# Optimization experiments

Measured on AMD Instinct MI355X. Metric: run time of the kernel, lower is better.

## Reference

```python
import jax, jax.numpy as jnp
import numpy as np

B, T, D, N = 2, 2048, 2048, 16
H = D // N          # 128 head dim
F = H // 2          # 64 rotary frequencies


def setup_inputs() -> dict:
    key = jax.random.key(0)
    k1, k2, k3 = jax.random.split(key, 3)
    x = jax.random.normal(k1, (B, T, D), dtype=jnp.float32)
    # causal mask [T, T], True = attend
    mask = jnp.tril(jnp.ones((T, T), dtype=bool))
    # RoPE tables: freqs = 1 / 10000^(2i/H), angles = t * freqs
    freqs = 1.0 / (10000.0 ** (jnp.arange(0, H, 2, dtype=jnp.float32) / H))  # [F]
    angles = jnp.arange(T, dtype=jnp.float32)[:, None] * freqs[None, :]      # [T, F]
    cos, sin = jnp.cos(angles), jnp.sin(angles)
    w_attn = jax.random.normal(k2, (D, 3 * D), dtype=jnp.float32) * 0.02
    w_out = jax.random.normal(k3, (D, D), dtype=jnp.float32) * 0.02
    return {"x": x, "mask": mask, "cos": cos, "sin": sin,
            "w_attn": w_attn, "w_out": w_out}


def _rope(x_BNTH, cos_TF, sin_TF):
    # complex multiply on adjacent pairs of the head dim
    x = x_BNTH.reshape(*x_BNTH.shape[:-1], F, 2)  # [B,N,T,F,2]
    xr, xi = x[..., 0], x[..., 1]
    out_r = xr * cos_TF - xi * sin_TF             # broadcast [T,F] over [B,N,T,F]
    out_i = xr * sin_TF + xi * cos_TF
    return jnp.stack([out_r, out_i], axis=-1).reshape(x_BNTH.shape)


def reference(x, mask, cos, sin, w_attn, w_out):
    qkv = x @ w_attn                                  # [B,T,3D]
    q, k, v = jnp.split(qkv, 3, axis=-1)
    def to_heads(z):
        return z.reshape(B, T, N, H).transpose(0, 2, 1, 3)  # [B,N,T,H]
    q, k, v = to_heads(q), to_heads(k), to_heads(v)
    # NOTE: this module applies rotary embedding to k AND v (not q), per source
    k = _rope(k, cos, sin)
    v = _rope(v, cos, sin)
    scale = 1.0 / jnp.sqrt(jnp.asarray(H, dtype=q.dtype))
    scores = jnp.einsum('bnqh,bnkh->bnqk', q, k) * scale  # [B,N,T,T]
    scores = jnp.where(mask, scores, jnp.finfo(scores.dtype).min)
    attn = jax.nn.softmax(scores, axis=-1)
    o = jnp.einsum('bnqk,bnkh->bnqh', attn, v)            # [B,N,T,H]
    o = o.transpose(0, 2, 1, 3).reshape(B, T, D)          # [B,T,D]
    return o @ w_out
```

## Files before the change

### kernel.cpp

```cpp
#include <hip/hip_runtime.h>

typedef unsigned short u16;
typedef unsigned int u32;

#define B_ 2
#define T_ 2048
#define D_ 2048
#define N_ 16
#define H_ 128
#define F_ 64
#define SCALE 0.08838834764831845f

typedef __attribute__((ext_vector_type(8))) __bf16 bf16x8;
typedef __attribute__((ext_vector_type(8))) short s16x8;
typedef __attribute__((ext_vector_type(4))) float f32x4;
typedef __attribute__((ext_vector_type(4))) u16 u16x4;

__device__ inline u16 f2bf(float f) {
    union { float f; u32 u; } v; v.f = f;
    u32 u = v.u;
    u32 r = (u + 0x7FFFu + ((u >> 16) & 1u)) >> 16;
    return (u16)r;
}
__device__ inline float bf2f(u16 h) {
    union { u32 u; float f; } v; v.u = ((u32)h) << 16;
    return v.f;
}
__device__ inline bf16x8 ld8(const u16* p) {
    s16x8 r = *reinterpret_cast<const s16x8*>(p);
    return __builtin_bit_cast(bf16x8, r);
}
__device__ inline f32x4 mfma16(bf16x8 a, bf16x8 b, f32x4 c) {
    return __builtin_amdgcn_mfma_f32_16x16x32_bf16(a, b, c, 0, 0, 0);
}
__device__ inline void gload_lds16(const u16* g, u16* l) {
    __builtin_amdgcn_global_load_lds(
        (const __attribute__((address_space(1))) void*)g,
        (__attribute__((address_space(3))) void*)l, 16, 0, 0);
}

__global__ __launch_bounds__(256) void cvt_bf16(const float* __restrict__ in,
                                                u16* __restrict__ out, int n) {
    int i = (blockIdx.x * 256 + threadIdx.x) * 8;
    if (i >= n) return;
    float4 a = *reinterpret_cast<const float4*>(in + i);
    float4 b = *reinterpret_cast<const float4*>(in + i + 4);
    s16x8 o;
    o[0] = (short)f2bf(a.x); o[1] = (short)f2bf(a.y);
    o[2] = (short)f2bf(a.z); o[3] = (short)f2bf(a.w);
    o[4] = (short)f2bf(b.x); o[5] = (short)f2bf(b.y);
    o[6] = (short)f2bf(b.z); o[7] = (short)f2bf(b.w);
    *reinterpret_cast<s16x8*>(out + i) = o;
}

__global__ __launch_bounds__(256) void transpose_cvt(const float* __restrict__ in,
                                                     u16* __restrict__ out,
                                                     int K, int Nc) {
    __shared__ float tile[64][65];
    int n0 = blockIdx.x * 64, k0 = blockIdx.y * 64;
    int tid = threadIdx.x;
    int rr = tid >> 4;
    int cc = (tid & 15) * 4;
#pragma unroll
    for (int it = 0; it < 4; ++it) {
        int kk = it * 16 + rr;
        float4 v = *reinterpret_cast<const float4*>(in + (size_t)(k0 + kk) * Nc + n0 + cc);
        tile[kk][cc] = v.x; tile[kk][cc + 1] = v.y; tile[kk][cc + 2] = v.z; tile[kk][cc + 3] = v.w;
    }
    __syncthreads();
#pragma unroll
    for (int it = 0; it < 4; ++it) {
        int nn = it * 16 + rr;
        u16x4 o;
#pragma unroll
        for (int j = 0; j < 4; ++j) o[j] = f2bf(tile[cc + j][nn]);
        *reinterpret_cast<u16x4*>(out + (size_t)(n0 + nn) * K + k0 + cc) = o;
    }
}

#define BM 128
#define BN 128
#define BKg 32

__global__ __launch_bounds__(256) void gemm_bt(const u16* __restrict__ A,
                                               const u16* __restrict__ Bt,
                                               u16* __restrict__ Cb,
                                               float* __restrict__ Cf,
                                               int M, int Nn, int K, int out_f32) {
    __shared__ __align__(16) u16 As[2][BM * BKg];
    __shared__ __align__(16) u16 Bs[2][BM * BKg];
    const int tid = threadIdx.x;
    const int wave = tid >> 6, lane = tid & 63;
    const int m0 = blockIdx.y * BM, n0 = blockIdx.x * BN;
    const int lrow = lane >> 2, lcol = (lane & 3) * 8;
    const int wr = (wave >> 1) * 64, wc = (wave & 1) * 64;
    const int g = lane >> 4, c0 = lane & 15;

    f32x4 acc[4][4] = {};

    const int NT = K / BKg;

    auto stage = [&](int buf, int kt) {
        const int k0 = kt * BKg;
#pragma unroll
        for (int j = 0; j < 2; ++j) {
            const int c = wave + j * 4;
            gload_lds16(A + (size_t)(m0 + c * 16 + lrow) * K + k0 + lcol, &As[buf][c * 512]);
            gload_lds16(Bt + (size_t)(n0 + c * 16 + lrow) * K + k0 + lcol, &Bs[buf][c * 512]);
        }
    };

    stage(0, 0);
    __syncthreads();

    for (int t = 0; t < NT; ++t) {
        const int cur = t & 1;
        if (t + 1 < NT) stage(cur ^ 1, t + 1);
        bf16x8 af[4], bfr[4];
#pragma unroll
        for (int i = 0; i < 4; ++i) {
            af[i]  = ld8(&As[cur][(wr + i * 16 + c0) * BKg + g * 8]);
            bfr[i] = ld8(&Bs[cur][(wc + i * 16 + c0) * BKg + g * 8]);
        }
#pragma unroll
        for (int i = 0; i < 4; ++i)
#pragma unroll
            for (int j = 0; j < 4; ++j)
                acc[i][j] = mfma16(af[i], bfr[j], acc[i][j]);
        __syncthreads();
    }

#pragma unroll
    for (int i = 0; i < 4; ++i)
#pragma unroll
        for (int j = 0; j < 4; ++j)
#pragma unroll
            for (int r = 0; r < 4; ++r) {
                int row = m0 + wr + i * 16 + g * 4 + r;
                int col = n0 + wc + j * 16 + c0;
                float v = acc[i][j][r];
                if (out_f32) Cf[(size_t)row * Nn + col] = v;
                else         Cb[(size_t)row * Nn + col] = f2bf(v);
            }
}

__global__ __launch_bounds__(256) void rope_split(const u16* __restrict__ qkv,
                                                  const float* __restrict__ cosT,
                                                  const float* __restrict__ sinT,
                                                  u16* __restrict__ qs,
                                                  u16* __restrict__ kr,
                                                  u16* __restrict__ vt) {
    __shared__ u16 vtile[64][129];
    int bi = blockIdx.x;
    int hn = bi >> 5;
    int tt = bi & 31;
    int b = hn >> 4, n = hn & 15;
    int t0 = tt * 64;
    int tid = threadIdx.x;
    int tl = tid >> 2;
    int h0 = (tid & 3) * 32;
    int t = t0 + tl;
    const u16* row = qkv + ((size_t)(b * T_ + t)) * (3 * D_);

#pragma unroll
    for (int u = 0; u < 4; ++u) {
        s16x8 raw = *reinterpret_cast<const s16x8*>(row + n * H_ + h0 + u * 8);
        s16x8 o;
#pragma unroll
        for (int e = 0; e < 8; ++e) o[e] = (short)f2bf(bf2f((u16)raw[e]) * SCALE);
        *reinterpret_cast<s16x8*>(qs + ((size_t)hn * T_ + t) * H_ + h0 + u * 8) = o;
    }

    float cbuf[16], sbuf[16];
    const float* cr = cosT + (size_t)t * F_ + h0 / 2;
    const float* sr = sinT + (size_t)t * F_ + h0 / 2;
#pragma unroll
    for (int u = 0; u < 4; ++u) {
        float4 c4 = *reinterpret_cast<const float4*>(cr + u * 4);
        float4 s4 = *reinterpret_cast<const float4*>(sr + u * 4);
        cbuf[u * 4 + 0] = c4.x; cbuf[u * 4 + 1] = c4.y; cbuf[u * 4 + 2] = c4.z; cbuf[u * 4 + 3] = c4.w;
        sbuf[u * 4 + 0] = s4.x; sbuf[u * 4 + 1] = s4.y; sbuf[u * 4 + 2] = s4.z; sbuf[u * 4 + 3] = s4.w;
    }

#pragma unroll
    for (int u = 0; u < 4; ++u) {
        s16x8 raw = *reinterpret_cast<const s16x8*>(row + D_ + n * H_ + h0 + u * 8);
        s16x8 o;
#pragma unroll
        for (int p = 0; p < 4; ++p) {
            float xr = bf2f((u16)raw[2 * p]), xi = bf2f((u16)raw[2 * p + 1]);
            float cc = cbuf[u * 4 + p], ss = sbuf[u * 4 + p];
            o[2 * p]     = (short)f2bf(xr * cc - xi * ss);
            o[2 * p + 1] = (short)f2bf(xr * ss + xi * cc);
        }
        *reinterpret_cast<s16x8*>(kr + ((size_t)hn * T_ + t) * H_ + h0 + u * 8) = o;
    }

#pragma unroll
    for (int u = 0; u < 4; ++u) {
        s16x8 raw = *reinterpret_cast<const s16x8*>(row + 2 * D_ + n * H_ + h0 + u * 8);
#pragma unroll
        for (int p = 0; p < 4; ++p) {
            float xr = bf2f((u16)raw[2 * p]), xi = bf2f((u16)raw[2 * p + 1]);
            float cc = cbuf[u * 4 + p], ss = sbuf[u * 4 + p];
            vtile[tl][h0 + u * 8 + 2 * p]     = f2bf(xr * cc - xi * ss);
            vtile[tl][h0 + u * 8 + 2 * p + 1] = f2bf(xr * ss + xi * cc);
        }
    }
    __syncthreads();

    int hrow = tid >> 1;
    int th = (tid & 1) * 32;
    u16 tmp[32];
#pragma unroll
    for (int i = 0; i < 32; ++i) tmp[i] = vtile[th + i][hrow];
    u16* dst = vt + ((size_t)(hn * H_ + hrow)) * T_ + t0 + th;
#pragma unroll
    for (int u = 0; u < 4; ++u) {
        s16x8 o;
#pragma unroll
        for (int e = 0; e < 8; ++e) o[e] = (short)tmp[u * 8 + e];
        *reinterpret_cast<s16x8*>(dst + u * 8) = o;
    }
}

__global__ __launch_bounds__(256, 2) void attn_fwd(const u16* __restrict__ qs,
                                                   const u16* __restrict__ kr,
                                                   const u16* __restrict__ vt,
                                                   u16* __restrict__ ob) {
    __shared__ __align__(16) u16 Ks[2][8192];
    __shared__ __align__(16) u16 Vs[2][8192];
    __shared__ __align__(16) u16 plds[4][2][1024];

    const int wave = threadIdx.x >> 6, lane = threadIdx.x & 63;
    const int g = lane >> 4, c0 = lane & 15;

    const int wg = blockIdx.x;
    const int orig = (wg & 7) * 64 + (wg >> 3);
    const int hn = orig >> 4;
    const int qt = orig & 15;
    const int bq0 = (15 - qt) * 128;

    const u16* qh = qs + (size_t)hn * T_ * H_;
    const u16* kh = kr + (size_t)hn * T_ * H_;
    const u16* vh = vt + (size_t)hn * H_ * T_;

    const int q0[2] = { bq0 + wave * 16, bq0 + 64 + wave * 16 };

    bf16x8 qf[2][4];
#pragma unroll
    for (int i = 0; i < 2; ++i)
#pragma unroll
        for (int kf = 0; kf < 4; ++kf)
            qf[i][kf] = ld8(qh + (size_t)(q0[i] + c0) * H_ + kf * 32 + g * 8);

    f32x4 o[2][8] = {};
    float m[2][4], l[2][4];
#pragma unroll
    for (int i = 0; i < 2; ++i)
#pragma unroll
        for (int r = 0; r < 4; ++r) { m[i][r] = -1e30f; l[i][r] = 0.0f; }

    const int nt = bq0 / 64 + 2;

    auto stage = [&](int buf, int t) {
        const int kv0 = t * 64;
#pragma unroll
        for (int j = 0; j < 4; ++j) {
            int ra = wave * 16 + j * 4 + (lane >> 4);
            int ca = ((lane & 15) * 8) ^ ((ra & 7) << 3);
            gload_lds16(kh + (size_t)(kv0 + ra) * H_ + ca, &Ks[buf][wave * 2048 + j * 512]);
            int rv = wave * 32 + j * 8 + (lane >> 3);
            int cv = ((lane & 7) * 8) ^ ((rv & 7) << 3);
            gload_lds16(vh + (size_t)rv * T_ + kv0 + cv, &Vs[buf][wave * 2048 + j * 512]);
        }
    };

    stage(0, 0);
    __syncthreads();

    for (int t = 0; t < nt; ++t) {
        const int cur = t & 1;
        const int kv0 = t * 64;
        if (t + 1 < nt) stage(cur ^ 1, t + 1);

        const bool a0 = kv0 < q0[0] + 16;
        const bool a1 = kv0 < q0[1] + 16;

        f32x4 s[2][4] = {};
#pragma unroll
        for (int cc = 0; cc < 4; ++cc) {
            const int krow = cc * 16 + c0;
#pragma unroll
            for (int kf = 0; kf < 4; ++kf) {
                bf16x8 kfr = ld8(&Ks[cur][krow * 128 + ((kf * 32 + g * 8) ^ ((krow & 7) << 3))]);
                if (a0) s[0][cc] = mfma16(qf[0][kf], kfr, s[0][cc]);
                if (a1) s[1][cc] = mfma16(qf[1][kf], kfr, s[1][cc]);
            }
        }

        bf16x8 pa[2][2];
#pragma unroll
        for (int i = 0; i < 2; ++i) {
            const bool act = i ? a1 : a0;
            if (!act) continue;
            if (kv0 + 63 > q0[i]) {
#pragma unroll
                for (int cc = 0; cc < 4; ++cc) {
                    int col = kv0 + cc * 16 + c0;
#pragma unroll
                    for (int r = 0; r < 4; ++r)
                        if (col > q0[i] + g * 4 + r) s[i][cc][r] = -1e30f;
                }
            }
            float pm[4];
#pragma unroll
            for (int r = 0; r < 4; ++r)
                pm[r] = fmaxf(fmaxf(s[i][0][r], s[i][1][r]), fmaxf(s[i][2][r], s[i][3][r]));
#pragma unroll
            for (int r = 0; r < 4; ++r) {
                pm[r] = fmaxf(pm[r], __shfl_xor(pm[r], 1));
                pm[r] = fmaxf(pm[r], __shfl_xor(pm[r], 2));
                pm[r] = fmaxf(pm[r], __shfl_xor(pm[r], 4));
                pm[r] = fmaxf(pm[r], __shfl_xor(pm[r], 8));
            }
            float al[4], rs[4];
#pragma unroll
            for (int r = 0; r < 4; ++r) {
                float mn = fmaxf(m[i][r], pm[r]);
                al[r] = __expf(m[i][r] - mn);
                m[i][r] = mn;
                rs[r] = 0.0f;
            }
#pragma unroll
            for (int cc = 0; cc < 4; ++cc)
#pragma unroll
                for (int r = 0; r < 4; ++r) {
                    float p = __expf(s[i][cc][r] - m[i][r]);
                    s[i][cc][r] = p;
                    rs[r] += p;
                }
#pragma unroll
            for (int r = 0; r < 4; ++r) {
                rs[r] += __shfl_xor(rs[r], 1);
                rs[r] += __shfl_xor(rs[r], 2);
                rs[r] += __shfl_xor(rs[r], 4);
                rs[r] += __shfl_xor(rs[r], 8);
                l[i][r] = l[i][r] * al[r] + rs[r];
            }
#pragma unroll
            for (int hf = 0; hf < 8; ++hf)
#pragma unroll
                for (int r = 0; r < 4; ++r) o[i][hf][r] *= al[r];

            u16* pw = &plds[wave][i][0];
#pragma unroll
            for (int cc = 0; cc < 4; ++cc)
#pragma unroll
                for (int r = 0; r < 4; ++r) {
                    int prow = g * 4 + r;
                    pw[prow * 64 + ((cc * 16 + c0) ^ ((prow & 7) << 3))] = f2bf(s[i][cc][r]);
                }
#pragma unroll
            for (int kf2 = 0; kf2 < 2; ++kf2)
                pa[i][kf2] = ld8(&pw[c0 * 64 + ((kf2 * 32 + g * 8) ^ ((c0 & 7) << 3))]);
        }

#pragma unroll
        for (int hf = 0; hf < 8; ++hf) {
            const int vrow = hf * 16 + c0;
#pragma unroll
            for (int kf2 = 0; kf2 < 2; ++kf2) {
                bf16x8 vfr = ld8(&Vs[cur][vrow * 64 + ((kf2 * 32 + g * 8) ^ ((vrow & 7) << 3))]);
                if (a0) o[0][hf] = mfma16(pa[0][kf2], vfr, o[0][hf]);
                if (a1) o[1][hf] = mfma16(pa[1][kf2], vfr, o[1][hf]);
            }
        }
        __syncthreads();
    }

    const int bb = hn >> 4, nn = hn & 15;
#pragma unroll
    for (int i = 0; i < 2; ++i) {
        float inv[4];
#pragma unroll
        for (int r = 0; r < 4; ++r) inv[r] = 1.0f / l[i][r];
#pragma unroll
        for (int hf = 0; hf < 8; ++hf)
#pragma unroll
            for (int r = 0; r < 4; ++r) {
                int t = q0[i] + g * 4 + r;
                ob[((size_t)(bb * T_ + t)) * D_ + nn * H_ + hf * 16 + c0] = f2bf(o[i][hf][r] * inv[r]);
            }
    }
}

extern "C" void kernel_launch(void* const* d_in, const int* in_sizes, int n_in,
                              void* d_out, int out_size, void* d_ws, size_t ws_size,
                              hipStream_t stream) {
    const float* x      = (const float*)d_in[0];
    const float* cosT   = (const float*)d_in[2];
    const float* sinT   = (const float*)d_in[3];
    const float* w_attn = (const float*)d_in[4];
    const float* w_out  = (const float*)d_in[5];
    float* out = (float*)d_out;

    char* ws = (char*)d_ws;
    u16* xb  = (u16*)(ws + 0);
    u16* wat = (u16*)(ws + 16777216);
    u16* wot = (u16*)(ws + 41943040);
    u16* qkv = (u16*)(ws + 50331648);
    u16* qsb = (u16*)(ws + 100663296);
    u16* krb = (u16*)(ws + 117440512);
    u16* vtb = (u16*)(ws + 134217728);
    u16* obf = (u16*)(ws + 0);

    cvt_bf16<<<(B_ * T_ * D_) / (256 * 8), 256, 0, stream>>>(x, xb, B_ * T_ * D_);
    transpose_cvt<<<dim3(3 * D_ / 64, D_ / 64), 256, 0, stream>>>(w_attn, wat, D_, 3 * D_);
    transpose_cvt<<<dim3(D_ / 64, D_ / 64), 256, 0, stream>>>(w_out, wot, D_, D_);
    gemm_bt<<<dim3(3 * D_ / BN, B_ * T_ / BM), 256, 0, stream>>>(xb, wat, qkv, nullptr,
                                                                 B_ * T_, 3 * D_, D_, 0);
    rope_split<<<B_ * N_ * (T_ / 64), 256, 0, stream>>>(qkv, cosT, sinT, qsb, krb, vtb);
    attn_fwd<<<B_ * N_ * (T_ / 128), 256, 0, stream>>>(qsb, krb, vtb, obf);
    gemm_bt<<<dim3(D_ / BN, B_ * T_ / BM), 256, 0, stream>>>(obf, wot, nullptr, out,
                                                             B_ * T_, D_, D_, 1);
}
```

Before: 369.6 us.

## Transpose attention MFMAs, use exp2 softmax with lazy rescale and register shuffles

The attention kernel swaps the MFMA operand order so each lane holds the scores of one query row. This lets the row max and sum stay per lane and cuts the cross-lane reductions. The Q prescale now folds in log2(e), so softmax uses the raw v_exp_f32 exp2 instruction, and the running max is only updated when the new max exceeds the old by more than 8 (log2 units). P is packed with v_cvt_pk_bf16_f32 and redistributed through lane shuffles instead of a round trip through LDS, and s_setprio raises priority around the MFMA blocks. Output stores become 4-wide vectors. The lazy rescale lets probabilities exceed 1 by up to 2^8 before the max is updated, which adds some risk of precision loss.

```diff
diff --git a/kernel.cpp b/kernel.cpp
--- a/kernel.cpp
+++ b/kernel.cpp
@@ -9,12 +9,13 @@
 #define N_ 16
 #define H_ 128
 #define F_ 64
-#define SCALE 0.08838834764831845f
+#define QSCALE 0.12751743226f
 
 typedef __attribute__((ext_vector_type(8))) __bf16 bf16x8;
 typedef __attribute__((ext_vector_type(8))) short s16x8;
 typedef __attribute__((ext_vector_type(4))) float f32x4;
 typedef __attribute__((ext_vector_type(4))) u16 u16x4;
+typedef __attribute__((ext_vector_type(4))) u32 u32x4;
 
 __device__ inline u16 f2bf(float f) {
     union { float f; u32 u; } v; v.f = f;
@@ -37,6 +38,16 @@
     __builtin_amdgcn_global_load_lds(
         (const __attribute__((address_space(1))) void*)g,
         (__attribute__((address_space(3))) void*)l, 16, 0, 0);
+}
+__device__ inline float exp2fast(float x) {
+    float r;
+    asm("v_exp_f32 %0, %1" : "=v"(r) : "v"(x));
+    return r;
+}
+__device__ inline u32 cvtpk(float lo, float hi) {
+    u32 r;
+    asm("v_cvt_pk_bf16_f32 %0, %1, %2" : "=v"(r) : "v"(lo), "v"(hi));
+    return r;
 }
 
 __global__ __launch_bounds__(256) void cvt_bf16(const float* __restrict__ in,
@@ -167,7 +178,7 @@
         s16x8 raw = *reinterpret_cast<const s16x8*>(row + n * H_ + h0 + u * 8);
         s16x8 o;
 #pragma unroll
-        for (int e = 0; e < 8; ++e) o[e] = (short)f2bf(bf2f((u16)raw[e]) * SCALE);
+        for (int e = 0; e < 8; ++e) o[e] = (short)f2bf(bf2f((u16)raw[e]) * QSCALE);
         *reinterpret_cast<s16x8*>(qs + ((size_t)hn * T_ + t) * H_ + h0 + u * 8) = o;
     }
 
@@ -230,7 +241,6 @@
                                                    u16* __restrict__ ob) {
     __shared__ __align__(16) u16 Ks[2][8192];
     __shared__ __align__(16) u16 Vs[2][8192];
-    __shared__ __align__(16) u16 plds[4][2][1024];
 
     const int wave = threadIdx.x >> 6, lane = threadIdx.x & 63;
     const int g = lane >> 4, c0 = lane & 15;
@@ -255,11 +265,8 @@
             qf[i][kf] = ld8(qh + (size_t)(q0[i] + c0) * H_ + kf * 32 + g * 8);
 
     f32x4 o[2][8] = {};
-    float m[2][4], l[2][4];
-#pragma unroll
-    for (int i = 0; i < 2; ++i)
-#pragma unroll
-        for (int r = 0; r < 4; ++r) { m[i][r] = -1e30f; l[i][r] = 0.0f; }
+    float m[2] = { -1e30f, -1e30f };
+    float l[2] = { 0.0f, 0.0f };
 
     const int nt = bq0 / 64 + 2;
 
@@ -279,6 +286,10 @@
     stage(0, 0);
     __syncthreads();
 
+    const int srcA = ((g & 1) * 2) * 16 + c0;
+    const int srcB = srcA + 16;
+    const int sel  = g >> 1;
+
     for (int t = 0; t < nt; ++t) {
         const int cur = t & 1;
         const int kv0 = t * 64;
@@ -288,110 +299,110 @@
         const bool a1 = kv0 < q0[1] + 16;
 
         f32x4 s[2][4] = {};
+        __builtin_amdgcn_s_setprio(1);
 #pragma unroll
         for (int cc = 0; cc < 4; ++cc) {
             const int krow = cc * 16 + c0;
 #pragma unroll
             for (int kf = 0; kf < 4; ++kf) {
                 bf16x8 kfr = ld8(&Ks[cur][krow * 128 + ((kf * 32 + g * 8) ^ ((krow & 7) << 3))]);
-                if (a0) s[0][cc] = mfma16(qf[0][kf], kfr, s[0][cc]);
-                if (a1) s[1][cc] = mfma16(qf[1][kf], kfr, s[1][cc]);
-            }
-        }
-
-        bf16x8 pa[2][2];
+                if (a0) s[0][cc] = mfma16(kfr, qf[0][kf], s[0][cc]);
+                if (a1) s[1][cc] = mfma16(kfr, qf[1][kf], s[1][cc]);
+            }
+        }
+        __builtin_amdgcn_s_setprio(0);
+
+        bf16x8 pb[2][2];
 #pragma unroll
         for (int i = 0; i < 2; ++i) {
             const bool act = i ? a1 : a0;
             if (!act) continue;
+            const int qrow = q0[i] + c0;
             if (kv0 + 63 > q0[i]) {
 #pragma unroll
                 for (int cc = 0; cc < 4; ++cc) {
-                    int col = kv0 + cc * 16 + c0;
+                    int kloc = kv0 + cc * 16 + g * 4;
 #pragma unroll
                     for (int r = 0; r < 4; ++r)
-                        if (col > q0[i] + g * 4 + r) s[i][cc][r] = -1e30f;
+                        if (kloc + r > qrow) s[i][cc][r] = -1e30f;
                 }
             }
-            float pm[4];
-#pragma unroll
-            for (int r = 0; r < 4; ++r)
-                pm[r] = fmaxf(fmaxf(s[i][0][r], s[i][1][r]), fmaxf(s[i][2][r], s[i][3][r]));
-#pragma unroll
-            for (int r = 0; r < 4; ++r) {
-                pm[r] = fmaxf(pm[r], __shfl_xor(pm[r], 1));
-                pm[r] = fmaxf(pm[r], __shfl_xor(pm[r], 2));
-                pm[r] = fmaxf(pm[r], __shfl_xor(pm[r], 4));
-                pm[r] = fmaxf(pm[r], __shfl_xor(pm[r], 8));
-            }
-            float al[4], rs[4];
-#pragma unroll
-            for (int r = 0; r < 4; ++r) {
-                float mn = fmaxf(m[i][r], pm[r]);
-                al[r] = __expf(m[i][r] - mn);
-                m[i][r] = mn;
-                rs[r] = 0.0f;
-            }
+            float pmax = s[i][0][0];
 #pragma unroll
             for (int cc = 0; cc < 4; ++cc)
 #pragma unroll
-                for (int r = 0; r < 4; ++r) {
-                    float p = __expf(s[i][cc][r] - m[i][r]);
-                    s[i][cc][r] = p;
-                    rs[r] += p;
-                }
-#pragma unroll
-            for (int r = 0; r < 4; ++r) {
-                rs[r] += __shfl_xor(rs[r], 1);
-                rs[r] += __shfl_xor(rs[r], 2);
-                rs[r] += __shfl_xor(rs[r], 4);
-                rs[r] += __shfl_xor(rs[r], 8);
-                l[i][r] = l[i][r] * al[r] + rs[r];
-            }
-#pragma unroll
-            for (int hf = 0; hf < 8; ++hf)
-#pragma unroll
-                for (int r = 0; r < 4; ++r) o[i][hf][r] *= al[r];
-
-            u16* pw = &plds[wave][i][0];
-#pragma unroll
-            for (int cc = 0; cc < 4; ++cc)
-#pragma unroll
-                for (int r = 0; r < 4; ++r) {
-                    int prow = g * 4 + r;
-                    pw[prow * 64 + ((cc * 16 + c0) ^ ((prow & 7) << 3))] = f2bf(s[i][cc][r]);
-                }
-#pragma unroll
-            for (int kf2 = 0; kf2 < 2; ++kf2)
-                pa[i][kf2] = ld8(&pw[c0 * 64 + ((kf2 * 32 + g * 8) ^ ((c0 & 7) << 3))]);
-        }
-
+                for (int r = 0; r < 4; ++r) pmax = fmaxf(pmax, s[i][cc][r]);
+            if (!__all(pmax <= m[i] + 8.0f)) {
+                pmax = fmaxf(pmax, __shfl_xor(pmax, 16));
+                pmax = fmaxf(pmax, __shfl_xor(pmax, 32));
+                float mn = fmaxf(m[i], pmax);
+                float al = exp2fast(m[i] - mn);
+                m[i] = mn;
+                l[i] *= al;
+#pragma unroll
+                for (int hf = 0; hf < 8; ++hf)
+#pragma unroll
+                    for (int r = 0; r < 4; ++r) o[i][hf][r] *= al;
+            }
+            u32 w[4][2];
+#pragma unroll
+            for (int cc = 0; cc < 4; ++cc) {
+                float p0 = exp2fast(s[i][cc][0] - m[i]);
+                float p1 = exp2fast(s[i][cc][1] - m[i]);
+                float p2 = exp2fast(s[i][cc][2] - m[i]);
+                float p3 = exp2fast(s[i][cc][3] - m[i]);
+                l[i] += (p0 + p1) + (p2 + p3);
+                w[cc][0] = cvtpk(p0, p1);
+                w[cc][1] = cvtpk(p2, p3);
+            }
+#pragma unroll
+            for (int ks2 = 0; ks2 < 2; ++ks2) {
+                u32 r00 = __shfl(w[ks2 * 2 + 0][0], srcA);
+                u32 r01 = __shfl(w[ks2 * 2 + 0][1], srcA);
+                u32 r02 = __shfl(w[ks2 * 2 + 0][0], srcB);
+                u32 r03 = __shfl(w[ks2 * 2 + 0][1], srcB);
+                u32 r10 = __shfl(w[ks2 * 2 + 1][0], srcA);
+                u32 r11 = __shfl(w[ks2 * 2 + 1][1], srcA);
+                u32 r12 = __shfl(w[ks2 * 2 + 1][0], srcB);
+                u32 r13 = __shfl(w[ks2 * 2 + 1][1], srcB);
+                u32x4 wv;
+                wv[0] = sel ? r10 : r00;
+                wv[1] = sel ? r11 : r01;
+                wv[2] = sel ? r12 : r02;
+                wv[3] = sel ? r13 : r03;
+                pb[i][ks2] = __builtin_bit_cast(bf16x8, wv);
+            }
+        }
+
+        __builtin_amdgcn_s_setprio(1);
 #pragma unroll
         for (int hf = 0; hf < 8; ++hf) {
             const int vrow = hf * 16 + c0;
 #pragma unroll
-            for (int kf2 = 0; kf2 < 2; ++kf2) {
-                bf16x8 vfr = ld8(&Vs[cur][vrow * 64 + ((kf2 * 32 + g * 8) ^ ((vrow & 7) << 3))]);
-                if (a0) o[0][hf] = mfma16(pa[0][kf2], vfr, o[0][hf]);
-                if (a1) o[1][hf] = mfma16(pa[1][kf2], vfr, o[1][hf]);
-            }
-        }
+            for (int ks2 = 0; ks2 < 2; ++ks2) {
+                bf16x8 vfr = ld8(&Vs[cur][vrow * 64 + ((ks2 * 32 + g * 8) ^ ((vrow & 7) << 3))]);
+                if (a0) o[0][hf] = mfma16(vfr, pb[0][ks2], o[0][hf]);
+                if (a1) o[1][hf] = mfma16(vfr, pb[1][ks2], o[1][hf]);
+            }
+        }
+        __builtin_amdgcn_s_setprio(0);
         __syncthreads();
     }
 
     const int bb = hn >> 4, nn = hn & 15;
 #pragma unroll
     for (int i = 0; i < 2; ++i) {
-        float inv[4];
-#pragma unroll
-        for (int r = 0; r < 4; ++r) inv[r] = 1.0f / l[i][r];
-#pragma unroll
-        for (int hf = 0; hf < 8; ++hf)
-#pragma unroll
-            for (int r = 0; r < 4; ++r) {
-                int t = q0[i] + g * 4 + r;
-                ob[((size_t)(bb * T_ + t)) * D_ + nn * H_ + hf * 16 + c0] = f2bf(o[i][hf][r] * inv[r]);
-            }
+        float lt = l[i] + __shfl_xor(l[i], 16);
+        lt += __shfl_xor(lt, 32);
+        float inv = 1.0f / lt;
+        const size_t rowoff = ((size_t)(bb * T_ + q0[i] + c0)) * D_ + nn * H_ + g * 4;
+#pragma unroll
+        for (int hf = 0; hf < 8; ++hf) {
+            u16x4 pk;
+#pragma unroll
+            for (int r = 0; r < 4; ++r) pk[r] = f2bf(o[i][hf][r] * inv);
+            *reinterpret_cast<u16x4*>(ob + rowoff + hf * 16) = pk;
+        }
     }
 }
 
```

Result: faster. 328.3 us (-11.2%).
